# Kernel tuning notes

Measured on AMD Instinct MI355X. Metric: run time of the kernel, lower is better.

Reference implementation:

```python
import jax, jax.numpy as jnp
import numpy as np

B, T1, S = 32, 129, 256
E, H, K, V, VOCAB = 512, 1024, 128, 128, 8000


def _lstm_cell(x, h, c, W_ih, W_hh, b):
    # PyTorch LSTMCell gate order: i, f, g, o
    gates = x @ W_ih.T + h @ W_hh.T + b  # [B, 4H]
    i, f, g, o = jnp.split(gates, 4, axis=-1)
    c_new = jax.nn.sigmoid(f) * c + jax.nn.sigmoid(i) * jnp.tanh(g)
    h_new = jax.nn.sigmoid(o) * jnp.tanh(c_new)
    return h_new, c_new


def setup_inputs() -> dict:
    key = jax.random.key(0)
    ks = jax.random.split(key, 16)
    w = lambda k, shp: (jax.random.normal(k, shp, dtype=jnp.float32) * 0.02)
    return {
        "decoder_inputs": jax.random.randint(ks[0], (B, T1), 0, VOCAB),
        "inputs_lens": jax.random.randint(ks[1], (B,), 0, T1 - 1),
        "encoder_hidden": jax.random.normal(ks[2], (B, H), dtype=jnp.float32),
        "encoder_keys": jax.random.normal(ks[3], (B, S, K), dtype=jnp.float32),
        "encoder_values": jax.random.normal(ks[4], (B, S, V), dtype=jnp.float32),
        "embedding": w(ks[5], (VOCAB, E)),
        "W_ih1": w(ks[6], (4 * H, E + V)),
        "W_hh1": w(ks[7], (4 * H, H)),
        "b1": jnp.zeros((4 * H,), dtype=jnp.float32),
        "W_ih2": w(ks[8], (4 * H, H)),
        "W_hh2": w(ks[9], (4 * H, H)),
        "b2": jnp.zeros((4 * H,), dtype=jnp.float32),
        "W_q": w(ks[10], (K, H)),
        "b_q": jnp.zeros((K,), dtype=jnp.float32),
        "W_out": w(ks[11], (VOCAB, H + V)),
        "b_out": jnp.zeros((VOCAB,), dtype=jnp.float32),
    }


def reference(decoder_inputs, inputs_lens, encoder_hidden, encoder_keys,
              encoder_values, embedding, W_ih1, W_hh1, b1, W_ih2, W_hh2, b2,
              W_q, b_q, W_out, b_out):
    T = decoder_inputs.shape[1] - 1  # max_len = inputs.size(1) - 1
    # Teacher-forced embeddings, gathered once: [T, B, E]
    emb = jnp.swapaxes(embedding[decoder_inputs[:, :T]], 0, 1)

    h1 = h2 = encoder_hidden
    c1 = c2 = jnp.zeros_like(encoder_hidden)
    context0 = jnp.zeros((encoder_hidden.shape[0], encoder_values.shape[-1]),
                         dtype=encoder_hidden.dtype)

    def step(carry, emb_t):
        h1, c1, h2, c2, context = carry
        x = jnp.concatenate([emb_t, context], axis=1)  # [B, E+V]
        h1, c1 = _lstm_cell(x, h1, c1, W_ih1, W_hh1, b1)
        h2, c2 = _lstm_cell(h1, h2, c2, W_ih2, W_hh2, b2)
        # Attention over encoder keys/values
        q = h2 @ W_q.T + b_q                               # [B, K]
        energy = jnp.einsum('bsk,bk->bs', encoder_keys, q)  # [B, S]
        attn = jax.nn.softmax(energy, axis=-1)
        context = jnp.einsum('bs,bsv->bv', attn, encoder_values)  # [B, V]
        logits = jnp.concatenate([h2, context], axis=1) @ W_out.T + b_out
        return (h1, c1, h2, c2, context), logits

    _, logits = jax.lax.scan(step, (h1, c1, h2, c2, context0), emb)
    return jnp.swapaxes(logits, 0, 1)  # [B, T, VOCAB]
```

## Files before the change

### kernel.cpp

```cpp
#include <hip/hip_runtime.h>
#include <hip/hip_bf16.h>
#include <cstddef>

#define BB    32
#define T1    129
#define TT    128
#define SS    256
#define EE    512
#define HH    1024
#define KK    128
#define VV    128
#define VOC   8000
#define VOCP  8064
#define KLOG  1152
#define NB2   128
#define NATT  32

typedef __bf16 bf16x8 __attribute__((ext_vector_type(8)));
typedef float  f32x4  __attribute__((ext_vector_type(4)));
typedef unsigned int u32x4 __attribute__((ext_vector_type(4)));
typedef int    i32x2  __attribute__((ext_vector_type(2)));

#define MFMA(a,b,c) __builtin_amdgcn_mfma_f32_16x16x32_bf16((a),(b),(c),0,0,0)
#define VMCNT0 do { asm volatile("s_waitcnt vmcnt(0)" ::: "memory"); \
                    __builtin_amdgcn_sched_barrier(0); } while (0)

__device__ __forceinline__ void cstore16(const void* p, u32x4 v) {
    asm volatile("global_store_dwordx4 %0, %1, off sc0 sc1" :: "v"(p), "v"(v) : "memory");
}
__device__ __forceinline__ void cstore4f(const float* p, float v) {
    asm volatile("global_store_dword %0, %1, off sc0 sc1" :: "v"(p), "v"(v) : "memory");
}
__device__ __forceinline__ void cstore4i(const int* p, int v) {
    asm volatile("global_store_dword %0, %1, off sc0 sc1" :: "v"(p), "v"(v) : "memory");
}

__device__ __forceinline__ void poll128(const int* flags, int target, int lane)
{
    const int* p = flags + lane * 2;
    for (;;) {
        i32x2 f;
        asm volatile("global_load_dwordx2 %0, %1, off sc0 sc1\n\ts_waitcnt vmcnt(0)"
                     : "=v"(f) : "v"(p) : "memory");
        if (__all(f.x >= target && f.y >= target)) break;
        __builtin_amdgcn_s_sleep(1);
    }
}
__device__ __forceinline__ void poll32(const int* flags, int target, int lane)
{
    const int* p = flags + (lane & 31);
    for (;;) {
        int f;
        asm volatile("global_load_dword %0, %1, off sc0 sc1\n\ts_waitcnt vmcnt(0)"
                     : "=v"(f) : "v"(p) : "memory");
        if (__all(f >= target)) break;
        __builtin_amdgcn_s_sleep(1);
    }
}

union bf8u { __hip_bfloat16 h[8]; bf16x8 v; };

__device__ __forceinline__ bf16x8 cvt8(float4 a, float4 b) {
    bf8u u;
    u.h[0] = __float2bfloat16(a.x); u.h[1] = __float2bfloat16(a.y);
    u.h[2] = __float2bfloat16(a.z); u.h[3] = __float2bfloat16(a.w);
    u.h[4] = __float2bfloat16(b.x); u.h[5] = __float2bfloat16(b.y);
    u.h[6] = __float2bfloat16(b.z); u.h[7] = __float2bfloat16(b.w);
    return u.v;
}
__device__ __forceinline__ float fsig(float x) { return 1.f / (1.f + __expf(-x)); }

__global__ void pack_wout(const float* __restrict__ W, __hip_bfloat16* __restrict__ Wp)
{
    int v = blockIdx.y;
    int k = blockIdx.x * 256 + threadIdx.x;
    if (k >= KLOG) return;
    float w = (v < VOC) ? W[(size_t)v * KLOG + k] : 0.f;
    Wp[(size_t)v * KLOG + k] = __float2bfloat16(w);
}

__global__ void init_state(const float* __restrict__ enc,
                           __hip_bfloat16* __restrict__ H1s,
                           __hip_bfloat16* __restrict__ H2s,
                           int* __restrict__ bar)
{
    int i = blockIdx.x * 256 + threadIdx.x;
    if (i < 1024) bar[i] = 0;
    if (i >= BB * HH) return;
    __hip_bfloat16 eb = __float2bfloat16(enc[i]);
    H1s[i] = eb;
    H2s[i] = eb;
}

__global__ void gather_emb(const int* __restrict__ tok, const float* __restrict__ emb,
                           __hip_bfloat16* __restrict__ Aemb)
{
    int bid = blockIdx.x;
    int t = bid >> 5, b = bid & 31;
    int id = tok[b * T1 + t];
    const float* er = emb + (size_t)id * EE;
    __hip_bfloat16* dst = Aemb + (size_t)bid * EE;
    for (int k = threadIdx.x; k < EE; k += 256)
        dst[k] = __float2bfloat16(er[k]);
}

__global__ __launch_bounds__(512, 2) void decoder_persistent(
    const float* __restrict__ Wih1, const float* __restrict__ Whh1, const float* __restrict__ b1v,
    const float* __restrict__ Wih2, const float* __restrict__ Whh2, const float* __restrict__ b2v,
    const float* __restrict__ Wq,   const float* __restrict__ bq,
    const float* __restrict__ keys, const float* __restrict__ vals,
    const __hip_bfloat16* __restrict__ Aemb,
    __hip_bfloat16* H1s, __hip_bfloat16* H2s, __hip_bfloat16* CTXs,
    float* h2fs, float* q_s, __hip_bfloat16* Alog, int* bar)
{
    const int bid = blockIdx.x;
    const int tid = threadIdx.x;
    const int w   = tid >> 6;
    const int cg  = w >> 2;
    const int kq  = w & 3;
    const int l   = tid & 63;
    const int l15 = l & 15, l4 = l >> 4;
    const int n0  = bid * 32 + cg * 16;

    int* flag1 = bar;
    int* flag2 = bar + 128;
    int* flagq = bar + 256;
    int* flagc = bar + 384;

    __shared__ float G[2][4][32][17];
    __shared__ alignas(16) __hip_bfloat16 hstage[32][8];
    __shared__ alignas(16) float hstagef[32][8];
    __shared__ alignas(16) __hip_bfloat16 cstage[128];
    __shared__ float qs[KK];
    __shared__ float esl[SS];
    __shared__ float red[512];
    __shared__ float wmx[4], wsm[4];

    extern __shared__ __hip_bfloat16 kvls[];
    __hip_bfloat16 (*kls)[SS] = (__hip_bfloat16(*)[SS])kvls;
    __hip_bfloat16 (*vls)[VV] = (__hip_bfloat16(*)[VV])(kvls + KK * SS);

    bf16x8 w1e[4], w1c, w1h[8], w2a[8], w2b[8];
    {
        const int col  = n0 + l15;
        const int orow = (col & 3) * HH + (col >> 2);
        #pragma unroll
        for (int s = 0; s < 4; ++s) {
            int k0 = kq * 128 + s * 32 + l4 * 8;
            const float* p0 = Wih1 + (size_t)orow * (EE + VV) + k0;
            w1e[s] = cvt8(*(const float4*)p0, *(const float4*)(p0 + 4));
        }
        {
            int k0 = kq * 32 + l4 * 8;
            const float* p0 = Wih1 + (size_t)orow * (EE + VV) + EE + k0;
            w1c = cvt8(*(const float4*)p0, *(const float4*)(p0 + 4));
        }
        #pragma unroll
        for (int s = 0; s < 8; ++s) {
            int k0 = kq * 256 + s * 32 + l4 * 8;
            const float* p1 = Whh1 + (size_t)orow * HH + k0;
            const float* p2 = Wih2 + (size_t)orow * HH + k0;
            const float* p3 = Whh2 + (size_t)orow * HH + k0;
            w1h[s] = cvt8(*(const float4*)p1, *(const float4*)(p1 + 4));
            w2a[s] = cvt8(*(const float4*)p2, *(const float4*)(p2 + 4));
            w2b[s] = cvt8(*(const float4*)p3, *(const float4*)(p3 + 4));
        }
    }

    float c1r = 0.f, c2r = 0.f;
    float gb1[4], gb2[4];
    {
        int jl = tid & 7;
        int j  = bid * 8 + jl;
        #pragma unroll
        for (int g = 0; g < 4; ++g) { gb1[g] = b1v[g * HH + j]; gb2[g] = b2v[g * HH + j]; }
    }

    if (bid < NATT) {
        for (int i = tid; i < SS * KK; i += 512) {
            int s = i >> 7, k = i & 127;
            kls[k][s] = __float2bfloat16(keys[((size_t)bid * SS + s) * KK + k]);
            vls[s][k] = __float2bfloat16(vals[((size_t)bid * SS + s) * VV + k]);
        }
        __syncthreads();
    }

    f32x4 acc1A = {0,0,0,0}, acc1B = {0,0,0,0}, acc2A = {0,0,0,0}, acc2B = {0,0,0,0};
    #pragma unroll
    for (int s = 0; s < 4; ++s) {
        int k0 = kq * 128 + s * 32 + l4 * 8;
        bf16x8 a0 = *(const bf16x8*)(Aemb + (size_t)l15 * EE + k0);
        bf16x8 a1 = *(const bf16x8*)(Aemb + (size_t)(16 + l15) * EE + k0);
        acc1A = MFMA(a0, w1e[s], acc1A);
        acc1B = MFMA(a1, w1e[s], acc1B);
    }
    #pragma unroll
    for (int s = 0; s < 8; ++s) {
        int k0 = kq * 256 + s * 32 + l4 * 8;
        bf16x8 a0 = *(const bf16x8*)(H1s + (size_t)l15 * HH + k0);
        bf16x8 a1 = *(const bf16x8*)(H1s + (size_t)(16 + l15) * HH + k0);
        acc1A = MFMA(a0, w1h[s], acc1A);
        acc1B = MFMA(a1, w1h[s], acc1B);
        bf16x8 b0 = *(const bf16x8*)(H2s + (size_t)l15 * HH + k0);
        bf16x8 b1 = *(const bf16x8*)(H2s + (size_t)(16 + l15) * HH + k0);
        acc2A = MFMA(b0, w2b[s], acc2A);
        acc2B = MFMA(b1, w2b[s], acc2B);
    }

    bf16x8 fA[8], fB[8];

    #pragma unroll 1
    for (int t = 0; t < TT; ++t) {
        const int rnd = t + 1;
        __hip_bfloat16* AlogT = Alog + (size_t)t * BB * KLOG;
        const __hip_bfloat16* H1t = H1s + (size_t)rnd * BB * HH;
        const __hip_bfloat16* H2t = H2s + (size_t)rnd * BB * HH;
        float* h2ft = h2fs + (size_t)rnd * BB * HH;
        float* qt   = q_s  + (size_t)rnd * BB * KK;

        if (t > 0) {
            const __hip_bfloat16* Ct = CTXs + (size_t)t * BB * VV;
            int k0 = kq * 32 + l4 * 8;
            bf16x8 a0 = *(const bf16x8*)(Ct + (size_t)l15 * VV + k0);
            bf16x8 a1 = *(const bf16x8*)(Ct + (size_t)(16 + l15) * VV + k0);
            acc1A = MFMA(a0, w1c, acc1A);
            acc1B = MFMA(a1, w1c, acc1B);
        }
        #pragma unroll
        for (int r = 0; r < 4; ++r) {
            G[cg][kq][l4 * 4 + r][l15]      = acc1A[r];
            G[cg][kq][16 + l4 * 4 + r][l15] = acc1B[r];
        }
        acc1A = (f32x4){0,0,0,0}; acc1B = (f32x4){0,0,0,0};
        __syncthreads();
        if (tid < 256) {
            int b = tid >> 3, jl = tid & 7;
            int cg2 = jl >> 2, cb = (jl & 3) * 4;
            float g0 = G[cg2][0][b][cb+0] + G[cg2][1][b][cb+0] + G[cg2][2][b][cb+0] + G[cg2][3][b][cb+0] + gb1[0];
            float g1 = G[cg2][0][b][cb+1] + G[cg2][1][b][cb+1] + G[cg2][2][b][cb+1] + G[cg2][3][b][cb+1] + gb1[1];
            float g2 = G[cg2][0][b][cb+2] + G[cg2][1][b][cb+2] + G[cg2][2][b][cb+2] + G[cg2][3][b][cb+2] + gb1[2];
            float g3 = G[cg2][0][b][cb+3] + G[cg2][1][b][cb+3] + G[cg2][2][b][cb+3] + G[cg2][3][b][cb+3] + gb1[3];
            c1r = fsig(g1) * c1r + fsig(g0) * tanhf(g2);
            float h = fsig(g3) * tanhf(c1r);
            hstage[tid >> 3][tid & 7] = __float2bfloat16(h);
        }
        __syncthreads();
        if (tid < 32)
            cstore16((void*)(H1t + (size_t)tid * HH + bid * 8), *(const u32x4*)&hstage[tid][0]);
        VMCNT0;
        if (tid == 0) cstore4i(&flag1[bid], rnd);
        if (w == 0) poll128(flag1, rnd, l);
        __syncthreads();

        #pragma unroll
        for (int s = 0; s < 8; ++s) {
            int k0 = kq * 256 + s * 32 + l4 * 8;
            fA[s] = *(const bf16x8*)(H1t + (size_t)l15 * HH + k0);
            fB[s] = *(const bf16x8*)(H1t + (size_t)(16 + l15) * HH + k0);
        }
        #pragma unroll
        for (int s = 0; s < 8; ++s) {
            acc2A = MFMA(fA[s], w2a[s], acc2A);
            acc2B = MFMA(fB[s], w2a[s], acc2B);
            acc1A = MFMA(fA[s], w1h[s], acc1A);
            acc1B = MFMA(fB[s], w1h[s], acc1B);
        }
        #pragma unroll
        for (int r = 0; r < 4; ++r) {
            G[cg][kq][l4 * 4 + r][l15]      = acc2A[r];
            G[cg][kq][16 + l4 * 4 + r][l15] = acc2B[r];
        }
        acc2A = (f32x4){0,0,0,0}; acc2B = (f32x4){0,0,0,0};
        __syncthreads();
        if (tid < 256) {
            int b = tid >> 3, jl = tid & 7;
            int cg2 = jl >> 2, cb = (jl & 3) * 4;
            float g0 = G[cg2][0][b][cb+0] + G[cg2][1][b][cb+0] + G[cg2][2][b][cb+0] + G[cg2][3][b][cb+0] + gb2[0];
            float g1 = G[cg2][0][b][cb+1] + G[cg2][1][b][cb+1] + G[cg2][2][b][cb+1] + G[cg2][3][b][cb+1] + gb2[1];
            float g2 = G[cg2][0][b][cb+2] + G[cg2][1][b][cb+2] + G[cg2][2][b][cb+2] + G[cg2][3][b][cb+2] + gb2[2];
            float g3 = G[cg2][0][b][cb+3] + G[cg2][1][b][cb+3] + G[cg2][2][b][cb+3] + G[cg2][3][b][cb+3] + gb2[3];
            c2r = fsig(g1) * c2r + fsig(g0) * tanhf(g2);
            float h = fsig(g3) * tanhf(c2r);
            hstage[b][jl]  = __float2bfloat16(h);
            hstagef[b][jl] = h;
        }
        __syncthreads();
        if (tid < 32) {
            u32x4 v = *(const u32x4*)&hstage[tid][0];
            cstore16((void*)(H2t + (size_t)tid * HH + bid * 8), v);
            *(u32x4*)(AlogT + (size_t)tid * KLOG + bid * 8) = v;
            cstore16(h2ft + (size_t)tid * HH + bid * 8,     *(const u32x4*)&hstagef[tid][0]);
            cstore16(h2ft + (size_t)tid * HH + bid * 8 + 4, *(const u32x4*)&hstagef[tid][4]);
        }
        VMCNT0;
        if (tid == 0) cstore4i(&flag2[bid], rnd);
        if (w == 0) poll128(flag2, rnd, l);
        __syncthreads();

        {
            int b = tid >> 4, c = tid & 15;
            const float4* wr = (const float4*)(Wq + (size_t)bid * HH + c * 64);
            const float4* hr = (const float4*)(h2ft + (size_t)b * HH + c * 64);
            float acc = 0.f;
            #pragma unroll
            for (int i = 0; i < 16; ++i) {
                float4 wv4 = wr[i];
                float4 hv4 = hr[i];
                acc += wv4.x*hv4.x + wv4.y*hv4.y + wv4.z*hv4.z + wv4.w*hv4.w;
            }
            #pragma unroll
            for (int off = 8; off > 0; off >>= 1) acc += __shfl_xor(acc, off);
            if (c == 0) cstore4f(&qt[b * KK + bid], acc);
        }
        VMCNT0;
        __syncthreads();
        if (tid == 0) cstore4i(&flagq[bid], rnd);

        #pragma unroll
        for (int s = 0; s < 8; ++s) {
            int k0 = kq * 256 + s * 32 + l4 * 8;
            fA[s] = *(const bf16x8*)(H2t + (size_t)l15 * HH + k0);
            fB[s] = *(const bf16x8*)(H2t + (size_t)(16 + l15) * HH + k0);
        }
        #pragma unroll
        for (int s = 0; s < 8; ++s) {
            acc2A = MFMA(fA[s], w2b[s], acc2A);
            acc2B = MFMA(fB[s], w2b[s], acc2B);
        }
        if (t + 1 < TT) {
            const __hip_bfloat16* An = Aemb + (size_t)(t + 1) * BB * EE;
            #pragma unroll
            for (int s = 0; s < 4; ++s) {
                int k0 = kq * 128 + s * 32 + l4 * 8;
                bf16x8 a0 = *(const bf16x8*)(An + (size_t)l15 * EE + k0);
                bf16x8 a1 = *(const bf16x8*)(An + (size_t)(16 + l15) * EE + k0);
                acc1A = MFMA(a0, w1e[s], acc1A);
                acc1B = MFMA(a1, w1e[s], acc1B);
            }
        }

        if (bid < NATT) {
            const int b = bid;
            if (w == 0) poll128(flagq, rnd, l);
            __syncthreads();
            if (tid < KK) qs[tid] = qt[b * KK + tid] + bq[tid];
            __syncthreads();
            float en = 0.f;
            if (tid < SS) {
                #pragma unroll 8
                for (int k = 0; k < KK; ++k)
                    en += __bfloat162float(kls[k][tid]) * qs[k];
            }
            if (w < 4) {
                float m = en;
                #pragma unroll
                for (int off = 32; off > 0; off >>= 1)
                    m = fmaxf(m, __shfl_xor(m, off));
                if (l == 0) wmx[w] = m;
            }
            __syncthreads();
            float mx = fmaxf(fmaxf(wmx[0], wmx[1]), fmaxf(wmx[2], wmx[3]));
            if (w < 4) {
                float p = __expf(en - mx);
                esl[tid] = p;
                float sm = p;
                #pragma unroll
                for (int off = 32; off > 0; off >>= 1)
                    sm += __shfl_xor(sm, off);
                if (l == 0) wsm[w] = sm;
            }
            __syncthreads();
            float inv = 1.f / (wsm[0] + wsm[1] + wsm[2] + wsm[3]);
            {
                int v = tid & 127, sh = tid >> 7;
                float acc = 0.f;
                #pragma unroll 4
                for (int i = 0; i < 64; ++i)
                    acc += esl[sh * 64 + i] * __bfloat162float(vls[sh * 64 + i][v]);
                red[tid] = acc;
            }
            __syncthreads();
            if (tid < VV) {
                float cv = (red[tid] + red[tid+128] + red[tid+256] + red[tid+384]) * inv;
                cstage[tid] = __float2bfloat16(cv);
            }
            __syncthreads();
            if (tid < 16) {
                u32x4 v = *(const u32x4*)&cstage[tid * 8];
                cstore16((void*)(CTXs + (size_t)rnd * BB * VV + (size_t)b * VV + tid * 8), v);
                *(u32x4*)(AlogT + (size_t)b * KLOG + HH + tid * 8) = v;
            }
            VMCNT0;
            if (tid == 0) cstore4i(&flagc[bid], rnd);
        }
        if (w == 0) poll32(flagc, rnd, l);
        __syncthreads();
    }
}

__global__ __launch_bounds__(256) void logits_gemm(
    const __hip_bfloat16* __restrict__ Alog,
    const __hip_bfloat16* __restrict__ W,
    const float* __restrict__ bout,
    float* __restrict__ out)
{
    int n0 = blockIdx.x * 128;
    int m0 = blockIdx.y * 128;
    int wv = threadIdx.x >> 6, l = threadIdx.x & 63;
    int l15 = l & 15, l4 = l >> 4;

    f32x4 acc[8][2] = {};
    const __hip_bfloat16* Ap = Alog + (size_t)(m0 + l15) * KLOG + l4 * 8;
    const __hip_bfloat16* Bp = W    + (size_t)(n0 + wv * 32 + l15) * KLOG + l4 * 8;

    for (int kt = 0; kt < KLOG; kt += 32) {
        bf16x8 b0 = *(const bf16x8*)(Bp + kt);
        bf16x8 b1 = *(const bf16x8*)(Bp + (size_t)16 * KLOG + kt);
        #pragma unroll
        for (int ms = 0; ms < 8; ++ms) {
            bf16x8 a = *(const bf16x8*)(Ap + (size_t)ms * 16 * KLOG + kt);
            acc[ms][0] = MFMA(a, b0, acc[ms][0]);
            acc[ms][1] = MFMA(a, b1, acc[ms][1]);
        }
    }
    #pragma unroll
    for (int ms = 0; ms < 8; ++ms)
        #pragma unroll
        for (int ns = 0; ns < 2; ++ns) {
            int col = n0 + wv * 32 + ns * 16 + l15;
            if (col < VOC) {
                float bias = bout[col];
                #pragma unroll
                for (int r = 0; r < 4; ++r) {
                    int m = m0 + ms * 16 + l4 * 4 + r;
                    int b = m & 31, t = m >> 5;
                    out[((size_t)b * TT + t) * VOC + col] = acc[ms][ns][r] + bias;
                }
            }
        }
}

extern "C" void kernel_launch(void* const* d_in, const int* in_sizes, int n_in,
                              void* d_out, int out_size, void* d_ws, size_t ws_size,
                              hipStream_t stream)
{
    (void)in_sizes; (void)n_in; (void)out_size; (void)ws_size;
    const int*   dec  = (const int*)  d_in[0];
    const float* enc  = (const float*)d_in[2];
    const float* keys = (const float*)d_in[3];
    const float* vals = (const float*)d_in[4];
    const float* emb  = (const float*)d_in[5];
    const float* Wih1 = (const float*)d_in[6];
    const float* Whh1 = (const float*)d_in[7];
    const float* b1   = (const float*)d_in[8];
    const float* Wih2 = (const float*)d_in[9];
    const float* Whh2 = (const float*)d_in[10];
    const float* b2   = (const float*)d_in[11];
    const float* Wq   = (const float*)d_in[12];
    const float* bq   = (const float*)d_in[13];
    const float* Wout = (const float*)d_in[14];
    const float* bout = (const float*)d_in[15];
    float* out = (float*)d_out;

    char* p = (char*)d_ws;
    __hip_bfloat16* WoutP = (__hip_bfloat16*)p; p += (size_t)VOCP * KLOG * 2;
    __hip_bfloat16* Alog  = (__hip_bfloat16*)p; p += (size_t)TT * BB * KLOG * 2;
    __hip_bfloat16* Aemb  = (__hip_bfloat16*)p; p += (size_t)TT * BB * EE * 2;
    __hip_bfloat16* H1s   = (__hip_bfloat16*)p; p += (size_t)(TT + 1) * BB * HH * 2;
    __hip_bfloat16* H2s   = (__hip_bfloat16*)p; p += (size_t)(TT + 1) * BB * HH * 2;
    __hip_bfloat16* CTXs  = (__hip_bfloat16*)p; p += (size_t)(TT + 1) * BB * VV * 2;
    float* h2fs = (float*)p; p += (size_t)(TT + 1) * BB * HH * 4;
    float* q_s  = (float*)p; p += (size_t)(TT + 1) * BB * KK * 4;
    int* bar = (int*)p; p += 4096;

    pack_wout  <<<dim3((KLOG + 255) / 256, VOCP), 256, 0, stream>>>(Wout, WoutP);
    init_state <<<dim3(128), 256, 0, stream>>>(enc, H1s, H2s, bar);
    gather_emb <<<dim3(TT * BB), 256, 0, stream>>>(dec, emb, Aemb);

    decoder_persistent<<<dim3(NB2), 512, KK * SS * 2 + SS * VV * 2, stream>>>(
        Wih1, Whh1, b1, Wih2, Whh2, b2, Wq, bq, keys, vals,
        Aemb, H1s, H2s, CTXs, h2fs, q_s, Alog, bar);

    logits_gemm<<<dim3(VOCP / 128, (BB * TT) / 128), 256, 0, stream>>>(Alog, WoutP, bout, out);
}
```

Before: 4.625 ms.

## Restructure decoder grid sync: per-wave flag polling, fold query projection into attention blocks

Removes the separate distributed query-projection phase and its flag barrier. Each attention block now computes its own q row locally from bf16 H2 and a pre-packed bf16 Wq. Per-wave polling on only the flags covering each wave's K slice replaces the block-wide poll plus __syncthreads. The context-flag wait moves to the start of the next step, and sleep is dropped from the spin loops. This shortens the serial critical path per timestep, at the cost of redundant Wq work in the 32 attention blocks, reduced q precision (bf16 h2/Wq), and heavier spin traffic.

```diff
diff --git a/kernel.cpp b/kernel.cpp
--- a/kernel.cpp
+++ b/kernel.cpp
@@ -28,14 +28,21 @@
 __device__ __forceinline__ void cstore16(const void* p, u32x4 v) {
     asm volatile("global_store_dwordx4 %0, %1, off sc0 sc1" :: "v"(p), "v"(v) : "memory");
 }
-__device__ __forceinline__ void cstore4f(const float* p, float v) {
-    asm volatile("global_store_dword %0, %1, off sc0 sc1" :: "v"(p), "v"(v) : "memory");
-}
 __device__ __forceinline__ void cstore4i(const int* p, int v) {
     asm volatile("global_store_dword %0, %1, off sc0 sc1" :: "v"(p), "v"(v) : "memory");
 }
 
-__device__ __forceinline__ void poll128(const int* flags, int target, int lane)
+__device__ __forceinline__ void poll32v(const int* flags, int target, int lane)
+{
+    const int* p = flags + (lane & 31);
+    for (;;) {
+        int f;
+        asm volatile("global_load_dword %0, %1, off sc0 sc1\n\ts_waitcnt vmcnt(0)"
+                     : "=v"(f) : "v"(p) : "memory");
+        if (__all(f >= target)) break;
+    }
+}
+__device__ __forceinline__ void poll128v(const int* flags, int target, int lane)
 {
     const int* p = flags + lane * 2;
     for (;;) {
@@ -43,18 +50,6 @@
         asm volatile("global_load_dwordx2 %0, %1, off sc0 sc1\n\ts_waitcnt vmcnt(0)"
                      : "=v"(f) : "v"(p) : "memory");
         if (__all(f.x >= target && f.y >= target)) break;
-        __builtin_amdgcn_s_sleep(1);
-    }
-}
-__device__ __forceinline__ void poll32(const int* flags, int target, int lane)
-{
-    const int* p = flags + (lane & 31);
-    for (;;) {
-        int f;
-        asm volatile("global_load_dword %0, %1, off sc0 sc1\n\ts_waitcnt vmcnt(0)"
-                     : "=v"(f) : "v"(p) : "memory");
-        if (__all(f >= target)) break;
-        __builtin_amdgcn_s_sleep(1);
     }
 }
 
@@ -79,6 +74,12 @@
     Wp[(size_t)v * KLOG + k] = __float2bfloat16(w);
 }
 
+__global__ void pack_wq(const float* __restrict__ Wq, __hip_bfloat16* __restrict__ WqP)
+{
+    int i = blockIdx.x * 256 + threadIdx.x;
+    WqP[i] = __float2bfloat16(Wq[i]);
+}
+
 __global__ void init_state(const float* __restrict__ enc,
                            __hip_bfloat16* __restrict__ H1s,
                            __hip_bfloat16* __restrict__ H2s,
@@ -107,11 +108,11 @@
 __global__ __launch_bounds__(512, 2) void decoder_persistent(
     const float* __restrict__ Wih1, const float* __restrict__ Whh1, const float* __restrict__ b1v,
     const float* __restrict__ Wih2, const float* __restrict__ Whh2, const float* __restrict__ b2v,
-    const float* __restrict__ Wq,   const float* __restrict__ bq,
+    const __hip_bfloat16* __restrict__ WqP, const float* __restrict__ bq,
     const float* __restrict__ keys, const float* __restrict__ vals,
     const __hip_bfloat16* __restrict__ Aemb,
     __hip_bfloat16* H1s, __hip_bfloat16* H2s, __hip_bfloat16* CTXs,
-    float* h2fs, float* q_s, __hip_bfloat16* Alog, int* bar)
+    __hip_bfloat16* Alog, int* bar)
 {
     const int bid = blockIdx.x;
     const int tid = threadIdx.x;
@@ -124,13 +125,12 @@
 
     int* flag1 = bar;
     int* flag2 = bar + 128;
-    int* flagq = bar + 256;
-    int* flagc = bar + 384;
+    int* flagc = bar + 256;
 
     __shared__ float G[2][4][32][17];
     __shared__ alignas(16) __hip_bfloat16 hstage[32][8];
-    __shared__ alignas(16) float hstagef[32][8];
     __shared__ alignas(16) __hip_bfloat16 cstage[128];
+    __shared__ alignas(16) float hs[HH];
     __shared__ float qs[KK];
     __shared__ float esl[SS];
     __shared__ float red[512];
@@ -215,10 +215,9 @@
         __hip_bfloat16* AlogT = Alog + (size_t)t * BB * KLOG;
         const __hip_bfloat16* H1t = H1s + (size_t)rnd * BB * HH;
         const __hip_bfloat16* H2t = H2s + (size_t)rnd * BB * HH;
-        float* h2ft = h2fs + (size_t)rnd * BB * HH;
-        float* qt   = q_s  + (size_t)rnd * BB * KK;
 
         if (t > 0) {
+            poll32v(flagc, t, l);
             const __hip_bfloat16* Ct = CTXs + (size_t)t * BB * VV;
             int k0 = kq * 32 + l4 * 8;
             bf16x8 a0 = *(const bf16x8*)(Ct + (size_t)l15 * VV + k0);
@@ -245,12 +244,13 @@
             hstage[tid >> 3][tid & 7] = __float2bfloat16(h);
         }
         __syncthreads();
-        if (tid < 32)
-            cstore16((void*)(H1t + (size_t)tid * HH + bid * 8), *(const u32x4*)&hstage[tid][0]);
-        VMCNT0;
-        if (tid == 0) cstore4i(&flag1[bid], rnd);
-        if (w == 0) poll128(flag1, rnd, l);
-        __syncthreads();
+        if (w == 0) {
+            if (l < 32)
+                cstore16((void*)(H1t + (size_t)l * HH + bid * 8), *(const u32x4*)&hstage[l][0]);
+            VMCNT0;
+            if (l == 0) cstore4i(&flag1[bid], rnd);
+        }
+        poll32v(flag1 + kq * 32, rnd, l);
 
         #pragma unroll
         for (int s = 0; s < 8; ++s) {
@@ -281,69 +281,67 @@
             float g3 = G[cg2][0][b][cb+3] + G[cg2][1][b][cb+3] + G[cg2][2][b][cb+3] + G[cg2][3][b][cb+3] + gb2[3];
             c2r = fsig(g1) * c2r + fsig(g0) * tanhf(g2);
             float h = fsig(g3) * tanhf(c2r);
-            hstage[b][jl]  = __float2bfloat16(h);
-            hstagef[b][jl] = h;
+            hstage[tid >> 3][tid & 7] = __float2bfloat16(h);
         }
         __syncthreads();
-        if (tid < 32) {
-            u32x4 v = *(const u32x4*)&hstage[tid][0];
-            cstore16((void*)(H2t + (size_t)tid * HH + bid * 8), v);
-            *(u32x4*)(AlogT + (size_t)tid * KLOG + bid * 8) = v;
-            cstore16(h2ft + (size_t)tid * HH + bid * 8,     *(const u32x4*)&hstagef[tid][0]);
-            cstore16(h2ft + (size_t)tid * HH + bid * 8 + 4, *(const u32x4*)&hstagef[tid][4]);
-        }
-        VMCNT0;
-        if (tid == 0) cstore4i(&flag2[bid], rnd);
-        if (w == 0) poll128(flag2, rnd, l);
-        __syncthreads();
-
-        {
-            int b = tid >> 4, c = tid & 15;
-            const float4* wr = (const float4*)(Wq + (size_t)bid * HH + c * 64);
-            const float4* hr = (const float4*)(h2ft + (size_t)b * HH + c * 64);
-            float acc = 0.f;
-            #pragma unroll
-            for (int i = 0; i < 16; ++i) {
-                float4 wv4 = wr[i];
-                float4 hv4 = hr[i];
-                acc += wv4.x*hv4.x + wv4.y*hv4.y + wv4.z*hv4.z + wv4.w*hv4.w;
-            }
-            #pragma unroll
-            for (int off = 8; off > 0; off >>= 1) acc += __shfl_xor(acc, off);
-            if (c == 0) cstore4f(&qt[b * KK + bid], acc);
-        }
-        VMCNT0;
-        __syncthreads();
-        if (tid == 0) cstore4i(&flagq[bid], rnd);
-
-        #pragma unroll
-        for (int s = 0; s < 8; ++s) {
-            int k0 = kq * 256 + s * 32 + l4 * 8;
-            fA[s] = *(const bf16x8*)(H2t + (size_t)l15 * HH + k0);
-            fB[s] = *(const bf16x8*)(H2t + (size_t)(16 + l15) * HH + k0);
-        }
-        #pragma unroll
-        for (int s = 0; s < 8; ++s) {
-            acc2A = MFMA(fA[s], w2b[s], acc2A);
-            acc2B = MFMA(fB[s], w2b[s], acc2B);
-        }
-        if (t + 1 < TT) {
-            const __hip_bfloat16* An = Aemb + (size_t)(t + 1) * BB * EE;
-            #pragma unroll
-            for (int s = 0; s < 4; ++s) {
-                int k0 = kq * 128 + s * 32 + l4 * 8;
-                bf16x8 a0 = *(const bf16x8*)(An + (size_t)l15 * EE + k0);
-                bf16x8 a1 = *(const bf16x8*)(An + (size_t)(16 + l15) * EE + k0);
-                acc1A = MFMA(a0, w1e[s], acc1A);
-                acc1B = MFMA(a1, w1e[s], acc1B);
-            }
+        if (w == 0) {
+            if (l < 32) {
+                u32x4 v = *(const u32x4*)&hstage[l][0];
+                cstore16((void*)(H2t + (size_t)l * HH + bid * 8), v);
+                *(u32x4*)(AlogT + (size_t)l * KLOG + bid * 8) = v;
+            }
+            VMCNT0;
+            if (l == 0) cstore4i(&flag2[bid], rnd);
         }
 
         if (bid < NATT) {
             const int b = bid;
-            if (w == 0) poll128(flagq, rnd, l);
+            poll128v(flag2, rnd, l);
+            bf16x8 hrow;
+            if (tid < 128)
+                hrow = *(const bf16x8*)(H2t + (size_t)b * HH + tid * 8);
+            #pragma unroll
+            for (int s = 0; s < 8; ++s) {
+                int k0 = kq * 256 + s * 32 + l4 * 8;
+                fA[s] = *(const bf16x8*)(H2t + (size_t)l15 * HH + k0);
+                fB[s] = *(const bf16x8*)(H2t + (size_t)(16 + l15) * HH + k0);
+            }
+            #pragma unroll
+            for (int s = 0; s < 8; ++s) {
+                acc2A = MFMA(fA[s], w2b[s], acc2A);
+                acc2B = MFMA(fB[s], w2b[s], acc2B);
+            }
+            if (t + 1 < TT) {
+                const __hip_bfloat16* An = Aemb + (size_t)(t + 1) * BB * EE;
+                #pragma unroll
+                for (int s = 0; s < 4; ++s) {
+                    int k0 = kq * 128 + s * 32 + l4 * 8;
+                    bf16x8 a0 = *(const bf16x8*)(An + (size_t)l15 * EE + k0);
+                    bf16x8 a1 = *(const bf16x8*)(An + (size_t)(16 + l15) * EE + k0);
+                    acc1A = MFMA(a0, w1e[s], acc1A);
+                    acc1B = MFMA(a1, w1e[s], acc1B);
+                }
+            }
+            if (tid < 128) {
+                #pragma unroll
+                for (int e = 0; e < 8; ++e) hs[tid * 8 + e] = (float)hrow[e];
+            }
             __syncthreads();
-            if (tid < KK) qs[tid] = qt[b * KK + tid] + bq[tid];
+            {
+                int kp = tid >> 2, qc = tid & 3;
+                const bf16x8* wr = (const bf16x8*)(WqP + (size_t)kp * HH + qc * 256);
+                const float* hh = hs + qc * 256;
+                float acc = 0.f;
+                #pragma unroll 8
+                for (int c = 0; c < 32; ++c) {
+                    bf16x8 wv = wr[c];
+                    #pragma unroll
+                    for (int e = 0; e < 8; ++e) acc += (float)wv[e] * hh[c * 8 + e];
+                }
+                acc += __shfl_xor(acc, 1);
+                acc += __shfl_xor(acc, 2);
+                if (qc == 0) qs[kp] = acc + bq[kp];
+            }
             __syncthreads();
             float en = 0.f;
             if (tid < SS) {
@@ -385,16 +383,40 @@
                 cstage[tid] = __float2bfloat16(cv);
             }
             __syncthreads();
-            if (tid < 16) {
-                u32x4 v = *(const u32x4*)&cstage[tid * 8];
-                cstore16((void*)(CTXs + (size_t)rnd * BB * VV + (size_t)b * VV + tid * 8), v);
-                *(u32x4*)(AlogT + (size_t)b * KLOG + HH + tid * 8) = v;
-            }
-            VMCNT0;
-            if (tid == 0) cstore4i(&flagc[bid], rnd);
-        }
-        if (w == 0) poll32(flagc, rnd, l);
-        __syncthreads();
+            if (w == 0) {
+                if (l < 16) {
+                    u32x4 v = *(const u32x4*)&cstage[l * 8];
+                    cstore16((void*)(CTXs + (size_t)rnd * BB * VV + (size_t)b * VV + l * 8), v);
+                    *(u32x4*)(AlogT + (size_t)b * KLOG + HH + l * 8) = v;
+                }
+                VMCNT0;
+                if (l == 0) cstore4i(&flagc[bid], rnd);
+            }
+        } else {
+            poll32v(flag2 + kq * 32, rnd, l);
+            #pragma unroll
+            for (int s = 0; s < 8; ++s) {
+                int k0 = kq * 256 + s * 32 + l4 * 8;
+                fA[s] = *(const bf16x8*)(H2t + (size_t)l15 * HH + k0);
+                fB[s] = *(const bf16x8*)(H2t + (size_t)(16 + l15) * HH + k0);
+            }
+            #pragma unroll
+            for (int s = 0; s < 8; ++s) {
+                acc2A = MFMA(fA[s], w2b[s], acc2A);
+                acc2B = MFMA(fB[s], w2b[s], acc2B);
+            }
+            if (t + 1 < TT) {
+                const __hip_bfloat16* An = Aemb + (size_t)(t + 1) * BB * EE;
+                #pragma unroll
+                for (int s = 0; s < 4; ++s) {
+                    int k0 = kq * 128 + s * 32 + l4 * 8;
+                    bf16x8 a0 = *(const bf16x8*)(An + (size_t)l15 * EE + k0);
+                    bf16x8 a1 = *(const bf16x8*)(An + (size_t)(16 + l15) * EE + k0);
+                    acc1A = MFMA(a0, w1e[s], acc1A);
+                    acc1B = MFMA(a1, w1e[s], acc1B);
+                }
+            }
+        }
     }
 }
 
@@ -469,17 +491,17 @@
     __hip_bfloat16* H1s   = (__hip_bfloat16*)p; p += (size_t)(TT + 1) * BB * HH * 2;
     __hip_bfloat16* H2s   = (__hip_bfloat16*)p; p += (size_t)(TT + 1) * BB * HH * 2;
     __hip_bfloat16* CTXs  = (__hip_bfloat16*)p; p += (size_t)(TT + 1) * BB * VV * 2;
-    float* h2fs = (float*)p; p += (size_t)(TT + 1) * BB * HH * 4;
-    float* q_s  = (float*)p; p += (size_t)(TT + 1) * BB * KK * 4;
+    __hip_bfloat16* WqP   = (__hip_bfloat16*)p; p += (size_t)KK * HH * 2;
     int* bar = (int*)p; p += 4096;
 
     pack_wout  <<<dim3((KLOG + 255) / 256, VOCP), 256, 0, stream>>>(Wout, WoutP);
+    pack_wq    <<<dim3(512), 256, 0, stream>>>(Wq, WqP);
     init_state <<<dim3(128), 256, 0, stream>>>(enc, H1s, H2s, bar);
     gather_emb <<<dim3(TT * BB), 256, 0, stream>>>(dec, emb, Aemb);
 
     decoder_persistent<<<dim3(NB2), 512, KK * SS * 2 + SS * VV * 2, stream>>>(
-        Wih1, Whh1, b1, Wih2, Whh2, b2, Wq, bq, keys, vals,
-        Aemb, H1s, H2s, CTXs, h2fs, q_s, Alog, bar);
+        Wih1, Whh1, b1, Wih2, Whh2, b2, WqP, bq, keys, vals,
+        Aemb, H1s, H2s, CTXs, Alog, bar);
 
     logits_gemm<<<dim3(VOCP / 128, (BB * TT) / 128), 256, 0, stream>>>(Alog, WoutP, bout, out);
 }
```

Result: slower. 4.748 ms (+2.6%).
